# Performance work log

Measured on AMD Instinct MI355X. Metric: run time of the kernel, lower is better.

Reference implementation:

```python
import jax, jax.numpy as jnp
import numpy as np

N_NODES = 50000
N_EDGES = 1600000
IN_FEAT = 48
OUT_FEAT = 48
NUM_RELS = 8


def setup_inputs() -> dict:
    key = jax.random.key(0)
    ks = jax.random.split(key, 9)
    # xavier-ish scale for relu gain
    s1 = float(np.sqrt(2.0) * np.sqrt(6.0 / (IN_FEAT + IN_FEAT)))
    s2 = float(np.sqrt(2.0) * np.sqrt(6.0 / (IN_FEAT + OUT_FEAT)))
    return {
        "inputs": jax.random.normal(ks[0], (N_NODES, IN_FEAT), dtype=jnp.float32),
        "norm": jax.random.uniform(ks[1], (N_EDGES, 1), dtype=jnp.float32),
        "weight1": jax.random.uniform(ks[2], (NUM_RELS, IN_FEAT, IN_FEAT), jnp.float32, -s1, s1),
        "weight2": jax.random.uniform(ks[3], (NUM_RELS, IN_FEAT, OUT_FEAT), jnp.float32, -s2, s2),
        "bias1": jax.random.normal(ks[4], (IN_FEAT,), dtype=jnp.float32) * 0.1,
        "bias2": jax.random.normal(ks[5], (OUT_FEAT,), dtype=jnp.float32) * 0.1,
        "src": jax.random.randint(ks[6], (N_EDGES,), 0, N_NODES, dtype=jnp.int64) if jax.config.jax_enable_x64 else jax.random.randint(ks[6], (N_EDGES,), 0, N_NODES).astype(jnp.int32),
        "dst": jax.random.randint(ks[7], (N_EDGES,), 0, N_NODES).astype(jnp.int32),
        "rel_type": jax.random.randint(ks[8], (N_EDGES,), 0, NUM_RELS).astype(jnp.int32),
    }


def reference(inputs, norm, weight1, weight2, bias1, bias2, src, dst, rel_type):
    # Message depends only on (src node, relation): precompute per (node, rel).
    # Stage 1: h1[n,r,:] = relu(h[n] @ W1[r] + b1)   -> [N, R, in]
    h1 = jax.nn.relu(jnp.einsum('ni,rij->nrj', inputs, weight1) + bias1)
    # Stage 2: h2[n,r,:] = h1[n,r] @ W2[r]           -> [N, R, out]
    h2 = jnp.einsum('nrj,rjo->nro', h1, weight2)
    # Per-edge gather + norm scaling                 -> [E, out]
    msg = h2[src, rel_type] * norm
    # Scatter-sum aggregation to destination nodes   -> [N, out]
    agg = jax.ops.segment_sum(msg, dst, num_segments=inputs.shape[0])
    # apply_func: bias2 + activation
    return jax.nn.relu(agg + bias2)
```

## Files before the change

### kernel.cpp

```cpp
#include <hip/hip_runtime.h>

#define NN 50000
#define EE 1600000
#define FF 48
#define RR 8
#define H2_ROW 64
#define LSTR 72
#define NSEG 8
#define SCAP 16

#define WB 8
#define ZB 391
#define K1GRID (WB + ZB)

#define H2TILES 391
#define H2BLKS (H2TILES * RR)
#define K2GRID (H2BLKS * 3)

typedef __attribute__((ext_vector_type(8))) short frag8;
typedef __attribute__((ext_vector_type(4))) float frag4f;

__device__ inline unsigned short bf16r(float f) {
    unsigned u = __float_as_uint(f);
    return (unsigned short)((u + 0x7FFFu + ((u >> 16) & 1u)) >> 16);
}
__device__ inline unsigned bf16pack2(float a, float b) {
    return (unsigned)bf16r(a) | ((unsigned)bf16r(b) << 16);
}
__device__ inline frag8 pack8(float4 a, float4 b) {
    union { frag8 f; unsigned u[4]; } r;
    r.u[0] = bf16pack2(a.x, a.y); r.u[1] = bf16pack2(a.z, a.w);
    r.u[2] = bf16pack2(b.x, b.y); r.u[3] = bf16pack2(b.z, b.w);
    return r.f;
}

__global__ __launch_bounds__(256) void pre_kernel(
    const float* __restrict__ W1, const float* __restrict__ W2,
    unsigned short* __restrict__ W1t, unsigned short* __restrict__ W2t,
    int* __restrict__ count)
{
    int b = blockIdx.x;
    if (b < WB) {
        int r = b;
        const float* w1 = W1 + (size_t)r * FF * FF;
        const float* w2 = W2 + (size_t)r * FF * FF;
        for (int idx = threadIdx.x; idx < 48 * 64; idx += 256) {
            int j = idx >> 6, k = idx & 63;
            W1t[(size_t)r * 48 * 64 + idx] = (k < FF) ? bf16r(w1[k * FF + j]) : (unsigned short)0;
            W2t[(size_t)r * 48 * 64 + idx] = (k < FF) ? bf16r(w2[k * FF + j]) : (unsigned short)0;
        }
        return;
    }
    int z = (b - WB) * 256 + threadIdx.x;
    if (z < 100000) ((int4*)count)[z] = make_int4(0, 0, 0, 0);
}

__global__ __launch_bounds__(256) void h2_place_kernel(
    const float* __restrict__ X, const unsigned short* __restrict__ W1t,
    const unsigned short* __restrict__ W2t, const float* __restrict__ B1,
    const int* __restrict__ srcv, const int* __restrict__ dstv,
    const int* __restrict__ relv, const float* __restrict__ norm,
    int* __restrict__ count, unsigned* __restrict__ payload,
    unsigned short* __restrict__ H2)
{
    __shared__ unsigned short h1s[128 * LSTR];
    int b = blockIdx.x;
    int bmod = b - (b / 3) * 3;
    if (bmod != 0) {
        int p = (b / 3) * 2 + bmod - 1;
        int e = p * 256 + threadIdx.x;
        if (e < EE) {
            int xcd;
            asm volatile("s_getreg_b32 %0, hwreg(HW_REG_XCC_ID)" : "=s"(xcd));
            xcd &= (NSEG - 1);
            int d = dstv[e];
            unsigned qn = (unsigned)(norm[e] * 8192.0f + 0.5f);
            if (qn > 8191u) qn = 8191u;
            unsigned rec = ((unsigned)(srcv[e] * 8 + relv[e]) << 13) | qn;
            int x = xcd;
            #pragma unroll 1
            for (int attempt = 0; attempt < NSEG; ++attempt) {
                int pos = atomicAdd(&count[x * NN + d], 1);
                if (pos < SCAP) {
                    payload[((size_t)x * NN + d) * SCAP + pos] = rec;
                    break;
                }
                x = (x + 1) & (NSEG - 1);
            }
        }
        return;
    }
    int h    = b / 3;
    int r    = h & 7;
    int tile = h >> 3;
    int tid  = threadIdx.x;
    int w    = tid >> 6, ln = tid & 63, q = ln >> 4, lq = ln & 15;
    int nb   = tile * 128 + w * 32;

    unsigned short* myh1 = &h1s[(w * 32) * LSTR];
    for (int i = ln; i < 32 * 12; i += 64) {
        int rr = i / 12, cs = i - rr * 12;
        *(unsigned*)&myh1[rr * LSTR + 48 + cs * 2] = 0;
    }

    int row0 = nb + lq;      if (row0 >= NN) row0 = NN - 1;
    int row1 = nb + 16 + lq; if (row1 >= NN) row1 = NN - 1;
    const float* x0 = X + (size_t)row0 * FF;
    const float* x1 = X + (size_t)row1 * FF;

    frag8 a00 = pack8(*(const float4*)(x0 + q * 8), *(const float4*)(x0 + q * 8 + 4));
    frag8 a10 = pack8(*(const float4*)(x1 + q * 8), *(const float4*)(x1 + q * 8 + 4));
    frag8 a01 = {0, 0, 0, 0, 0, 0, 0, 0};
    frag8 a11 = {0, 0, 0, 0, 0, 0, 0, 0};
    if (q < 2) {
        a01 = pack8(*(const float4*)(x0 + 32 + q * 8), *(const float4*)(x0 + 36 + q * 8));
        a11 = pack8(*(const float4*)(x1 + 32 + q * 8), *(const float4*)(x1 + 36 + q * 8));
    }

    const unsigned short* w1r = W1t + (size_t)r * 48 * 64;
    const unsigned short* w2r = W2t + (size_t)r * 48 * 64;

    #pragma unroll
    for (int t = 0; t < 3; ++t) {
        int col = t * 16 + lq;
        frag8 b0 = *(const frag8*)&w1r[(col << 6) + q * 8];
        frag8 b1 = *(const frag8*)&w1r[(col << 6) + 32 + q * 8];
        float bc = B1[col];
        frag4f acc0 = {bc, bc, bc, bc};
        frag4f acc1 = {bc, bc, bc, bc};
        acc0 = __builtin_amdgcn_mfma_f32_16x16x32_bf16(a00, b0, acc0, 0, 0, 0);
        acc0 = __builtin_amdgcn_mfma_f32_16x16x32_bf16(a01, b1, acc0, 0, 0, 0);
        acc1 = __builtin_amdgcn_mfma_f32_16x16x32_bf16(a10, b0, acc1, 0, 0, 0);
        acc1 = __builtin_amdgcn_mfma_f32_16x16x32_bf16(a11, b1, acc1, 0, 0, 0);
        #pragma unroll
        for (int g = 0; g < 4; ++g) {
            myh1[(q * 4 + g) * LSTR + col]      = bf16r(fmaxf(acc0[g], 0.0f));
            myh1[(16 + q * 4 + g) * LSTR + col] = bf16r(fmaxf(acc1[g], 0.0f));
        }
    }

    const frag8 c00 = *(const frag8*)&myh1[lq * LSTR + q * 8];
    const frag8 c01 = *(const frag8*)&myh1[lq * LSTR + 32 + q * 8];
    const frag8 c10 = *(const frag8*)&myh1[(16 + lq) * LSTR + q * 8];
    const frag8 c11 = *(const frag8*)&myh1[(16 + lq) * LSTR + 32 + q * 8];

    #pragma unroll
    for (int t = 0; t < 3; ++t) {
        int col = t * 16 + lq;
        frag8 b0 = *(const frag8*)&w2r[(col << 6) + q * 8];
        frag8 b1 = *(const frag8*)&w2r[(col << 6) + 32 + q * 8];
        frag4f acc0 = {0.f, 0.f, 0.f, 0.f};
        frag4f acc1 = {0.f, 0.f, 0.f, 0.f};
        acc0 = __builtin_amdgcn_mfma_f32_16x16x32_bf16(c00, b0, acc0, 0, 0, 0);
        acc0 = __builtin_amdgcn_mfma_f32_16x16x32_bf16(c01, b1, acc0, 0, 0, 0);
        acc1 = __builtin_amdgcn_mfma_f32_16x16x32_bf16(c10, b0, acc1, 0, 0, 0);
        acc1 = __builtin_amdgcn_mfma_f32_16x16x32_bf16(c11, b1, acc1, 0, 0, 0);
        #pragma unroll
        for (int g = 0; g < 4; ++g) {
            int n0 = nb + q * 4 + g;
            int n1 = nb + 16 + q * 4 + g;
            if (n0 < NN)
                __builtin_nontemporal_store(bf16r(acc0[g]),
                    &H2[((size_t)n0 * RR + r) * H2_ROW + col]);
            if (n1 < NN)
                __builtin_nontemporal_store(bf16r(acc1[g]),
                    &H2[((size_t)n1 * RR + r) * H2_ROW + col]);
        }
    }
}

__global__ __launch_bounds__(256) void gather_kernel(
    const unsigned short* __restrict__ H2, const unsigned* __restrict__ payload,
    const int* __restrict__ count, const float* __restrict__ B2,
    float* __restrict__ out)
{
    unsigned tid = blockIdx.x * 256u + threadIdx.x;
    unsigned n = tid / 12u;
    unsigned c = tid - n * 12u;
    if (n >= NN) return;

    int cx[NSEG];
    #pragma unroll
    for (int x = 0; x < NSEG; ++x) cx[x] = min(count[(size_t)x * NN + n], SCAP);
    int p1 = cx[0], p2 = p1 + cx[1], p3 = p2 + cx[2], p4 = p3 + cx[3];
    int p5 = p4 + cx[4], p6 = p5 + cx[5], p7 = p6 + cx[6];
    int total = p7 + cx[7];
    const unsigned* pl = payload + (size_t)n * SCAP;

    auto slot = [&](int idx) -> unsigned {
        int x, base;
        if (idx < p4) {
            if (idx < p2) { x = (idx < p1) ? 0 : 1; base = (idx < p1) ? 0 : p1; }
            else          { x = (idx < p3) ? 2 : 3; base = (idx < p3) ? p2 : p3; }
        } else {
            if (idx < p6) { x = (idx < p5) ? 4 : 5; base = (idx < p5) ? p4 : p5; }
            else          { x = (idx < p7) ? 6 : 7; base = (idx < p7) ? p6 : p7; }
        }
        return pl[(size_t)x * (NN * SCAP) + (idx - base)];
    };

    float a0 = 0.f, a1 = 0.f, a2 = 0.f, a3 = 0.f;
    int e = 0;
    for (; e + 8 <= total; e += 8) {
        unsigned p[8];
        #pragma unroll
        for (int k = 0; k < 8; ++k) p[k] = slot(e + k);
        uint2 v[8];
        #pragma unroll
        for (int k = 0; k < 8; ++k)
            v[k] = ((const uint2*)(H2 + (size_t)(p[k] >> 13) * H2_ROW))[c];
        #pragma unroll
        for (int k = 0; k < 8; ++k) {
            float nm = (float)(p[k] & 8191u) * (1.0f / 8192.0f);
            a0 = fmaf(__uint_as_float(v[k].x << 16),         nm, a0);
            a1 = fmaf(__uint_as_float(v[k].x & 0xFFFF0000u), nm, a1);
            a2 = fmaf(__uint_as_float(v[k].y << 16),         nm, a2);
            a3 = fmaf(__uint_as_float(v[k].y & 0xFFFF0000u), nm, a3);
        }
    }
    for (; e < total; ++e) {
        unsigned p = slot(e);
        float nm = (float)(p & 8191u) * (1.0f / 8192.0f);
        uint2 v = ((const uint2*)(H2 + (size_t)(p >> 13) * H2_ROW))[c];
        a0 = fmaf(__uint_as_float(v.x << 16),         nm, a0);
        a1 = fmaf(__uint_as_float(v.x & 0xFFFF0000u), nm, a1);
        a2 = fmaf(__uint_as_float(v.y << 16),         nm, a2);
        a3 = fmaf(__uint_as_float(v.y & 0xFFFF0000u), nm, a3);
    }
    float4 b = ((const float4*)B2)[c];
    ((float4*)out)[(size_t)n * 12u + c] = make_float4(
        fmaxf(a0 + b.x, 0.f), fmaxf(a1 + b.y, 0.f),
        fmaxf(a2 + b.z, 0.f), fmaxf(a3 + b.w, 0.f));
}

extern "C" void kernel_launch(void* const* d_in, const int* in_sizes, int n_in,
                              void* d_out, int out_size, void* d_ws, size_t ws_size,
                              hipStream_t stream) {
    const float* X   = (const float*)d_in[0];
    const float* nrm = (const float*)d_in[1];
    const float* W1  = (const float*)d_in[2];
    const float* W2  = (const float*)d_in[3];
    const float* B1  = (const float*)d_in[4];
    const float* B2  = (const float*)d_in[5];
    const int*   src = (const int*)d_in[6];
    const int*   dst = (const int*)d_in[7];
    const int*   rel = (const int*)d_in[8];
    float* out = (float*)d_out;

    unsigned short* H2      = (unsigned short*)d_ws;
    unsigned*       payload = (unsigned*)(H2 + (size_t)NN * RR * H2_ROW);
    unsigned short* W1t     = (unsigned short*)(payload + (size_t)NN * NSEG * SCAP);
    unsigned short* W2t     = W1t + RR * 48 * 64;
    int*            count   = (int*)(W2t + RR * 48 * 64);

    pre_kernel<<<K1GRID, 256, 0, stream>>>(W1, W2, W1t, W2t, count);

    h2_place_kernel<<<K2GRID, 256, 0, stream>>>(
        X, W1t, W2t, B1, src, dst, rel, nrm, count, payload, H2);

    unsigned total = (unsigned)NN * 12u;
    gather_kernel<<<(total + 255) / 256, 256, 0, stream>>>(
        H2, payload, count, B2, out);
}
```

Baseline: 211.5 us.

## Compact H2 rows to 48 and loop relations per tile with staged vector stores

Removes the padding in the per-(node,relation) H2 rows, shrinking them from 64 to 48 bf16 values, which cuts the bytes written and the cache-line footprint of gathers. Each H2 block now loops over all 8 relations for its 128-node tile, reusing the loaded X fragments instead of reloading them per relation. Pairs of relation outputs are staged in shared memory and written with 16-byte nontemporal stores, replacing scattered 2-byte stores. The cost is fewer, longer-running H2 blocks. The placement blocks also no longer interleave with the H2 blocks in the grid.

```diff
diff --git a/kernel.cpp b/kernel.cpp
--- a/kernel.cpp
+++ b/kernel.cpp
@@ -4,7 +4,7 @@
 #define EE 1600000
 #define FF 48
 #define RR 8
-#define H2_ROW 64
+#define H2R 48
 #define LSTR 72
 #define NSEG 8
 #define SCAP 16
@@ -14,11 +14,12 @@
 #define K1GRID (WB + ZB)
 
 #define H2TILES 391
-#define H2BLKS (H2TILES * RR)
-#define K2GRID (H2BLKS * 3)
+#define PB ((EE + 255) / 256)
+#define K2GRID (H2TILES + PB)
 
 typedef __attribute__((ext_vector_type(8))) short frag8;
 typedef __attribute__((ext_vector_type(4))) float frag4f;
+typedef __attribute__((ext_vector_type(4))) unsigned uint4v;
 
 __device__ inline unsigned short bf16r(float f) {
     unsigned u = __float_as_uint(f);
@@ -63,12 +64,11 @@
     int* __restrict__ count, unsigned* __restrict__ payload,
     unsigned short* __restrict__ H2)
 {
-    __shared__ unsigned short h1s[128 * LSTR];
+    __shared__ __align__(16) unsigned short h1s[128 * LSTR];
+    __shared__ __align__(16) unsigned short h2s[128 * 96];
     int b = blockIdx.x;
-    int bmod = b - (b / 3) * 3;
-    if (bmod != 0) {
-        int p = (b / 3) * 2 + bmod - 1;
-        int e = p * 256 + threadIdx.x;
+    if (b >= H2TILES) {
+        int e = (b - H2TILES) * 256 + threadIdx.x;
         if (e < EE) {
             int xcd;
             asm volatile("s_getreg_b32 %0, hwreg(HW_REG_XCC_ID)" : "=s"(xcd));
@@ -90,14 +90,12 @@
         }
         return;
     }
-    int h    = b / 3;
-    int r    = h & 7;
-    int tile = h >> 3;
     int tid  = threadIdx.x;
     int w    = tid >> 6, ln = tid & 63, q = ln >> 4, lq = ln & 15;
-    int nb   = tile * 128 + w * 32;
+    int nb   = b * 128 + w * 32;
 
     unsigned short* myh1 = &h1s[(w * 32) * LSTR];
+    unsigned short* myh2 = &h2s[w * 32 * 96];
     for (int i = ln; i < 32 * 12; i += 64) {
         int rr = i / 12, cs = i - rr * 12;
         *(unsigned*)&myh1[rr * LSTR + 48 + cs * 2] = 0;
@@ -117,54 +115,69 @@
         a11 = pack8(*(const float4*)(x1 + 32 + q * 8), *(const float4*)(x1 + 36 + q * 8));
     }
 
-    const unsigned short* w1r = W1t + (size_t)r * 48 * 64;
-    const unsigned short* w2r = W2t + (size_t)r * 48 * 64;
-
-    #pragma unroll
-    for (int t = 0; t < 3; ++t) {
-        int col = t * 16 + lq;
-        frag8 b0 = *(const frag8*)&w1r[(col << 6) + q * 8];
-        frag8 b1 = *(const frag8*)&w1r[(col << 6) + 32 + q * 8];
-        float bc = B1[col];
-        frag4f acc0 = {bc, bc, bc, bc};
-        frag4f acc1 = {bc, bc, bc, bc};
-        acc0 = __builtin_amdgcn_mfma_f32_16x16x32_bf16(a00, b0, acc0, 0, 0, 0);
-        acc0 = __builtin_amdgcn_mfma_f32_16x16x32_bf16(a01, b1, acc0, 0, 0, 0);
-        acc1 = __builtin_amdgcn_mfma_f32_16x16x32_bf16(a10, b0, acc1, 0, 0, 0);
-        acc1 = __builtin_amdgcn_mfma_f32_16x16x32_bf16(a11, b1, acc1, 0, 0, 0);
-        #pragma unroll
-        for (int g = 0; g < 4; ++g) {
-            myh1[(q * 4 + g) * LSTR + col]      = bf16r(fmaxf(acc0[g], 0.0f));
-            myh1[(16 + q * 4 + g) * LSTR + col] = bf16r(fmaxf(acc1[g], 0.0f));
-        }
-    }
-
-    const frag8 c00 = *(const frag8*)&myh1[lq * LSTR + q * 8];
-    const frag8 c01 = *(const frag8*)&myh1[lq * LSTR + 32 + q * 8];
-    const frag8 c10 = *(const frag8*)&myh1[(16 + lq) * LSTR + q * 8];
-    const frag8 c11 = *(const frag8*)&myh1[(16 + lq) * LSTR + 32 + q * 8];
-
-    #pragma unroll
-    for (int t = 0; t < 3; ++t) {
-        int col = t * 16 + lq;
-        frag8 b0 = *(const frag8*)&w2r[(col << 6) + q * 8];
-        frag8 b1 = *(const frag8*)&w2r[(col << 6) + 32 + q * 8];
-        frag4f acc0 = {0.f, 0.f, 0.f, 0.f};
-        frag4f acc1 = {0.f, 0.f, 0.f, 0.f};
-        acc0 = __builtin_amdgcn_mfma_f32_16x16x32_bf16(c00, b0, acc0, 0, 0, 0);
-        acc0 = __builtin_amdgcn_mfma_f32_16x16x32_bf16(c01, b1, acc0, 0, 0, 0);
-        acc1 = __builtin_amdgcn_mfma_f32_16x16x32_bf16(c10, b0, acc1, 0, 0, 0);
-        acc1 = __builtin_amdgcn_mfma_f32_16x16x32_bf16(c11, b1, acc1, 0, 0, 0);
-        #pragma unroll
-        for (int g = 0; g < 4; ++g) {
-            int n0 = nb + q * 4 + g;
-            int n1 = nb + 16 + q * 4 + g;
-            if (n0 < NN)
-                __builtin_nontemporal_store(bf16r(acc0[g]),
-                    &H2[((size_t)n0 * RR + r) * H2_ROW + col]);
-            if (n1 < NN)
-                __builtin_nontemporal_store(bf16r(acc1[g]),
-                    &H2[((size_t)n1 * RR + r) * H2_ROW + col]);
+    float bcv[3] = {B1[lq], B1[16 + lq], B1[32 + lq]};
+
+    #pragma unroll 1
+    for (int kp = 0; kp < 4; ++kp) {
+        #pragma unroll
+        for (int p = 0; p < 2; ++p) {
+            int r = (kp << 1) + p;
+            const unsigned short* w1r = W1t + (size_t)r * 48 * 64;
+            const unsigned short* w2r = W2t + (size_t)r * 48 * 64;
+
+            #pragma unroll
+            for (int t = 0; t < 3; ++t) {
+                int col = t * 16 + lq;
+                frag8 b0 = *(const frag8*)&w1r[(col << 6) + q * 8];
+                frag8 b1 = *(const frag8*)&w1r[(col << 6) + 32 + q * 8];
+                float bc = bcv[t];
+                frag4f acc0 = {bc, bc, bc, bc};
+                frag4f acc1 = {bc, bc, bc, bc};
+                acc0 = __builtin_amdgcn_mfma_f32_16x16x32_bf16(a00, b0, acc0, 0, 0, 0);
+                acc0 = __builtin_amdgcn_mfma_f32_16x16x32_bf16(a01, b1, acc0, 0, 0, 0);
+                acc1 = __builtin_amdgcn_mfma_f32_16x16x32_bf16(a10, b0, acc1, 0, 0, 0);
+                acc1 = __builtin_amdgcn_mfma_f32_16x16x32_bf16(a11, b1, acc1, 0, 0, 0);
+                #pragma unroll
+                for (int g = 0; g < 4; ++g) {
+                    myh1[(q * 4 + g) * LSTR + col]      = bf16r(fmaxf(acc0[g], 0.0f));
+                    myh1[(16 + q * 4 + g) * LSTR + col] = bf16r(fmaxf(acc1[g], 0.0f));
+                }
+            }
+
+            const frag8 c00 = *(const frag8*)&myh1[lq * LSTR + q * 8];
+            const frag8 c01 = *(const frag8*)&myh1[lq * LSTR + 32 + q * 8];
+            const frag8 c10 = *(const frag8*)&myh1[(16 + lq) * LSTR + q * 8];
+            const frag8 c11 = *(const frag8*)&myh1[(16 + lq) * LSTR + 32 + q * 8];
+
+            #pragma unroll
+            for (int t = 0; t < 3; ++t) {
+                int col = t * 16 + lq;
+                frag8 b0 = *(const frag8*)&w2r[(col << 6) + q * 8];
+                frag8 b1 = *(const frag8*)&w2r[(col << 6) + 32 + q * 8];
+                frag4f acc0 = {0.f, 0.f, 0.f, 0.f};
+                frag4f acc1 = {0.f, 0.f, 0.f, 0.f};
+                acc0 = __builtin_amdgcn_mfma_f32_16x16x32_bf16(c00, b0, acc0, 0, 0, 0);
+                acc0 = __builtin_amdgcn_mfma_f32_16x16x32_bf16(c01, b1, acc0, 0, 0, 0);
+                acc1 = __builtin_amdgcn_mfma_f32_16x16x32_bf16(c10, b0, acc1, 0, 0, 0);
+                acc1 = __builtin_amdgcn_mfma_f32_16x16x32_bf16(c11, b1, acc1, 0, 0, 0);
+                #pragma unroll
+                for (int g = 0; g < 4; ++g) {
+                    myh2[(q * 4 + g) * 96 + p * 48 + col]      = bf16r(acc0[g]);
+                    myh2[(16 + q * 4 + g) * 96 + p * 48 + col] = bf16r(acc1[g]);
+                }
+            }
+        }
+        #pragma unroll
+        for (int i6 = 0; i6 < 6; ++i6) {
+            int fl    = i6 * 64 + ln;
+            int row   = fl / 12;
+            int piece = fl - row * 12;
+            int n     = nb + row;
+            if (n < NN) {
+                uint4v v = *(const uint4v*)&myh2[fl * 8];
+                __builtin_nontemporal_store(v,
+                    (uint4v*)(H2 + ((size_t)n * RR + kp * 2) * H2R) + piece);
+            }
         }
     }
 }
@@ -208,7 +221,7 @@
         uint2 v[8];
         #pragma unroll
         for (int k = 0; k < 8; ++k)
-            v[k] = ((const uint2*)(H2 + (size_t)(p[k] >> 13) * H2_ROW))[c];
+            v[k] = ((const uint2*)(H2 + (size_t)(p[k] >> 13) * H2R))[c];
         #pragma unroll
         for (int k = 0; k < 8; ++k) {
             float nm = (float)(p[k] & 8191u) * (1.0f / 8192.0f);
@@ -221,16 +234,16 @@
     for (; e < total; ++e) {
         unsigned p = slot(e);
         float nm = (float)(p & 8191u) * (1.0f / 8192.0f);
-        uint2 v = ((const uint2*)(H2 + (size_t)(p >> 13) * H2_ROW))[c];
+        uint2 v = ((const uint2*)(H2 + (size_t)(p >> 13) * H2R))[c];
         a0 = fmaf(__uint_as_float(v.x << 16),         nm, a0);
         a1 = fmaf(__uint_as_float(v.x & 0xFFFF0000u), nm, a1);
         a2 = fmaf(__uint_as_float(v.y << 16),         nm, a2);
         a3 = fmaf(__uint_as_float(v.y & 0xFFFF0000u), nm, a3);
     }
-    float4 b = ((const float4*)B2)[c];
+    float4 bbb = ((const float4*)B2)[c];
     ((float4*)out)[(size_t)n * 12u + c] = make_float4(
-        fmaxf(a0 + b.x, 0.f), fmaxf(a1 + b.y, 0.f),
-        fmaxf(a2 + b.z, 0.f), fmaxf(a3 + b.w, 0.f));
+        fmaxf(a0 + bbb.x, 0.f), fmaxf(a1 + bbb.y, 0.f),
+        fmaxf(a2 + bbb.z, 0.f), fmaxf(a3 + bbb.w, 0.f));
 }
 
 extern "C" void kernel_launch(void* const* d_in, const int* in_sizes, int n_in,
@@ -248,7 +261,7 @@
     float* out = (float*)d_out;
 
     unsigned short* H2      = (unsigned short*)d_ws;
-    unsigned*       payload = (unsigned*)(H2 + (size_t)NN * RR * H2_ROW);
+    unsigned*       payload = (unsigned*)(H2 + (size_t)NN * RR * H2R);
     unsigned short* W1t     = (unsigned short*)(payload + (size_t)NN * NSEG * SCAP);
     unsigned short* W2t     = W1t + RR * 48 * 64;
     int*            count   = (int*)(W2t + RR * 48 * 64);
```

Measured after the change: 233.9 us. +10.6%, slower.

## Store H2 relation-major with unpadded 48-wide rows via LDS-staged vector stores

Applied to the files above, without the earlier changes.

Changes the H2 intermediate layout from node-major rows padded to 64 to relation-major rows of 48 bf16, with payload records encoding rel*NN+src. Each block's MFMA outputs are staged through LDS and written out as contiguous 16-byte vector stores instead of scattered 2-byte nontemporal stores. This reduces H2 footprint and write traffic. Gathers are no longer grouped by source node across relations, which may change cache locality. The staging reuses the h1 shared buffer, so correctness depends on every wave having finished its h1 reads before the overwrite.

```diff
diff --git a/kernel.cpp b/kernel.cpp
--- a/kernel.cpp
+++ b/kernel.cpp
@@ -4,7 +4,7 @@
 #define EE 1600000
 #define FF 48
 #define RR 8
-#define H2_ROW 64
+#define H2R 48
 #define LSTR 72
 #define NSEG 8
 #define SCAP 16
@@ -19,6 +19,7 @@
 
 typedef __attribute__((ext_vector_type(8))) short frag8;
 typedef __attribute__((ext_vector_type(4))) float frag4f;
+typedef __attribute__((ext_vector_type(4))) unsigned uint4v;
 
 __device__ inline unsigned short bf16r(float f) {
     unsigned u = __float_as_uint(f);
@@ -63,7 +64,7 @@
     int* __restrict__ count, unsigned* __restrict__ payload,
     unsigned short* __restrict__ H2)
 {
-    __shared__ unsigned short h1s[128 * LSTR];
+    __shared__ __align__(16) unsigned short h1s[128 * LSTR];
     int b = blockIdx.x;
     int bmod = b - (b / 3) * 3;
     if (bmod != 0) {
@@ -76,7 +77,7 @@
             int d = dstv[e];
             unsigned qn = (unsigned)(norm[e] * 8192.0f + 0.5f);
             if (qn > 8191u) qn = 8191u;
-            unsigned rec = ((unsigned)(srcv[e] * 8 + relv[e]) << 13) | qn;
+            unsigned rec = ((unsigned)(relv[e] * NN + srcv[e]) << 13) | qn;
             int x = xcd;
             #pragma unroll 1
             for (int attempt = 0; attempt < NSEG; ++attempt) {
@@ -157,15 +158,18 @@
         acc1 = __builtin_amdgcn_mfma_f32_16x16x32_bf16(c11, b1, acc1, 0, 0, 0);
         #pragma unroll
         for (int g = 0; g < 4; ++g) {
-            int n0 = nb + q * 4 + g;
-            int n1 = nb + 16 + q * 4 + g;
-            if (n0 < NN)
-                __builtin_nontemporal_store(bf16r(acc0[g]),
-                    &H2[((size_t)n0 * RR + r) * H2_ROW + col]);
-            if (n1 < NN)
-                __builtin_nontemporal_store(bf16r(acc1[g]),
-                    &H2[((size_t)n1 * RR + r) * H2_ROW + col]);
-        }
+            myh1[(q * 4 + g) * 48 + col]      = bf16r(acc0[g]);
+            myh1[(16 + q * 4 + g) * 48 + col] = bf16r(acc1[g]);
+        }
+    }
+
+    unsigned short* dst = H2 + ((size_t)r * NN + nb) * H2R;
+    #pragma unroll
+    for (int i3 = 0; i3 < 3; ++i3) {
+        int fl = i3 * 64 + ln;
+        int n  = nb + fl / 6;
+        if (n < NN)
+            *(uint4v*)(dst + fl * 8) = *(const uint4v*)&myh1[fl * 8];
     }
 }
 
@@ -208,7 +212,7 @@
         uint2 v[8];
         #pragma unroll
         for (int k = 0; k < 8; ++k)
-            v[k] = ((const uint2*)(H2 + (size_t)(p[k] >> 13) * H2_ROW))[c];
+            v[k] = ((const uint2*)(H2 + (size_t)(p[k] >> 13) * H2R))[c];
         #pragma unroll
         for (int k = 0; k < 8; ++k) {
             float nm = (float)(p[k] & 8191u) * (1.0f / 8192.0f);
@@ -221,16 +225,16 @@
     for (; e < total; ++e) {
         unsigned p = slot(e);
         float nm = (float)(p & 8191u) * (1.0f / 8192.0f);
-        uint2 v = ((const uint2*)(H2 + (size_t)(p >> 13) * H2_ROW))[c];
+        uint2 v = ((const uint2*)(H2 + (size_t)(p >> 13) * H2R))[c];
         a0 = fmaf(__uint_as_float(v.x << 16),         nm, a0);
         a1 = fmaf(__uint_as_float(v.x & 0xFFFF0000u), nm, a1);
         a2 = fmaf(__uint_as_float(v.y << 16),         nm, a2);
         a3 = fmaf(__uint_as_float(v.y & 0xFFFF0000u), nm, a3);
     }
-    float4 b = ((const float4*)B2)[c];
+    float4 bbb = ((const float4*)B2)[c];
     ((float4*)out)[(size_t)n * 12u + c] = make_float4(
-        fmaxf(a0 + b.x, 0.f), fmaxf(a1 + b.y, 0.f),
-        fmaxf(a2 + b.z, 0.f), fmaxf(a3 + b.w, 0.f));
+        fmaxf(a0 + bbb.x, 0.f), fmaxf(a1 + bbb.y, 0.f),
+        fmaxf(a2 + bbb.z, 0.f), fmaxf(a3 + bbb.w, 0.f));
 }
 
 extern "C" void kernel_launch(void* const* d_in, const int* in_sizes, int n_in,
@@ -248,7 +252,7 @@
     float* out = (float*)d_out;
 
     unsigned short* H2      = (unsigned short*)d_ws;
-    unsigned*       payload = (unsigned*)(H2 + (size_t)NN * RR * H2_ROW);
+    unsigned*       payload = (unsigned*)(H2 + (size_t)NN * RR * H2R);
     unsigned short* W1t     = (unsigned short*)(payload + (size_t)NN * NSEG * SCAP);
     unsigned short* W2t     = W1t + RR * 48 * 64;
     int*            count   = (int*)(W2t + RR * 48 * 64);
```

Result: slower. 219.5 us (+3.8%).
